# Kernel tuning notes

Hardware: AMD Instinct MI355X
Metric: run time of the kernel (lower is better)

The kernel has to match this reference:

```python
import jax, jax.numpy as jnp
import numpy as np

L, B, S, D = 8, 1, 4096, 2048
H, KVH, HD = 16, 2, 128
Q = 32
THETA = 1e6
MROPE = (16, 24, 24)  # mrope_section, sums to HD//2
EPS = 1e-6


def setup_inputs() -> dict:
    key = jax.random.key(0)
    ks = jax.random.split(key, 8)
    hidden_states = jax.random.normal(ks[0], (L, B, S, D), dtype=jnp.float32)
    ln_w = jax.random.uniform(ks[1], (L, D), dtype=jnp.float32, minval=0.5, maxval=1.5)
    q_w = jax.random.normal(ks[2], (L, D, H * HD), dtype=jnp.float32) * 0.02
    q_b = jax.random.normal(ks[3], (L, H * HD), dtype=jnp.float32) * 0.02
    k_w = jax.random.normal(ks[4], (L, D, KVH * HD), dtype=jnp.float32) * 0.02
    k_b = jax.random.normal(ks[5], (L, KVH * HD), dtype=jnp.float32) * 0.02
    position_ids = jax.random.randint(ks[6], (3, B, S), 0, S, dtype=jnp.int32)
    q_idx = jnp.sort(jax.random.randint(ks[7], (Q,), 0, S, dtype=jnp.int32))
    return {"hidden_states": hidden_states, "ln_w": ln_w, "q_w": q_w, "q_b": q_b,
            "k_w": k_w, "k_b": k_b, "position_ids": position_ids, "q_idx": q_idx}


def _rot_half(x):
    h = x.shape[-1] // 2
    return jnp.concatenate([-x[..., h:], x[..., :h]], axis=-1)


def _mrope_combine(t):
    # t: (3, B, S, HD). Split last dim per 2*mrope_section, chunk i taken from axis i%3.
    parts, off = [], 0
    for i, sec in enumerate(MROPE):
        w = 2 * sec
        parts.append(t[i % 3, :, :, off:off + w])
        off += w
    return jnp.concatenate(parts, axis=-1)[:, None, :, :]  # (B, 1, S, HD)


def reference(hidden_states, ln_w, q_w, q_b, k_w, k_b, position_ids, q_idx):
    # Rotary embeddings from 3D mRoPE position ids
    inv_freq = 1.0 / (THETA ** (jnp.arange(0, HD, 2, dtype=jnp.float32) / HD))  # (HD/2,)
    freqs = position_ids.astype(jnp.float32)[..., None] * inv_freq  # (3, B, S, HD/2)
    emb = jnp.concatenate([freqs, freqs], axis=-1)  # (3, B, S, HD)
    cos = _mrope_combine(jnp.cos(emb))  # (B, 1, S, HD)
    sin = _mrope_combine(jnp.sin(emb))
    cos_q = cos[:, :, q_idx, :]  # (B, 1, Q, HD)
    sin_q = sin[:, :, q_idx, :]
    # Eager causal mask sliced at query rows: (Q, S)
    mask_add = jnp.where(jnp.arange(S)[None, :] > q_idx[:, None], -1e9, 0.0).astype(jnp.float32)

    scale = 1.0 / np.sqrt(HD).astype(np.float32)

    def per_layer(hs, lw, qw, qb, kw, kb):
        # RMSNorm (input_layernorm)
        var = jnp.mean(jnp.square(hs), axis=-1, keepdims=True)
        x = hs * jax.lax.rsqrt(var + EPS) * lw  # (B, S, D)
        xq = x[:, q_idx, :]  # (B, Q, D)
        k = (jnp.einsum('bsd,de->bse', x, kw) + kb).reshape(B, S, KVH, HD).transpose(0, 2, 1, 3)
        q = (jnp.einsum('bqd,de->bqe', xq, qw) + qb).reshape(B, Q, H, HD).transpose(0, 2, 1, 3)
        k = jnp.repeat(k, H // KVH, axis=1)  # repeat_kv -> (B, H, S, HD)
        k = k * cos + _rot_half(k) * sin
        q = q * cos_q + _rot_half(q) * sin_q
        scores = jnp.einsum('bhqd,bhkd->bhqk', q, k) * scale  # (B, H, Q, S)
        scores = scores + mask_add[None, None]
        return jax.nn.softmax(scores.astype(jnp.float32), axis=-1)

    return jax.vmap(per_layer)(hidden_states, ln_w, q_w, q_b, k_w, k_b)  # (L, B, H, Q, S)
```

## Files before the change

### kernel.cpp

```cpp
#include <hip/hip_runtime.h>
#include <hip/hip_bf16.h>
#include <math.h>

#define LYR 8
#define SEQ 4096
#define DIM 2048
#define NH 16
#define HD 128
#define NQ 32
#define NKV 256
#define NQE 2048

typedef __attribute__((ext_vector_type(8))) short short8;
typedef __attribute__((ext_vector_type(4))) float f32x4;

#define WS_ABLOB 256
#define WS_COS   524544
#define WS_SIN   1048832
#define WS_PART  2097408
#define WS_W2    6291712
#define WS_KBLOB 10486016
#define WS_QROPE 18874624

__device__ __forceinline__ short f2bf(float x) {
  __hip_bfloat16 h = __float2bfloat16(x);
  return *(short*)&h;
}
__device__ __forceinline__ float bf2f(short s) {
  unsigned u = ((unsigned)(unsigned short)s) << 16;
  return __uint_as_float(u);
}

__device__ __forceinline__ void split1(float x, short& h, short& l) {
  unsigned b = __float_as_uint(x);
  h = (short)(b >> 16);
  float lo = x - __uint_as_float(b & 0xffff0000u);
  l = (short)((__float_as_uint(lo) + 0x8000u) >> 16);
}

#define GLOAD16(srcp, dstp) \
  __builtin_amdgcn_global_load_lds( \
      (const __attribute__((address_space(1))) unsigned int*)(srcp), \
      (__attribute__((address_space(3))) unsigned int*)(dstp), 16, 0, 0)

#define RBAR() asm volatile("s_waitcnt lgkmcnt(0)\n\ts_barrier" ::: "memory")

__global__ __launch_bounds__(256) void prep_kernel(
    const float* __restrict__ ln_w, const float* __restrict__ k_w,
    short* __restrict__ W2) {
  int kb = blockIdx.x, l = blockIdx.y, t = threadIdx.x;
  const float* kwl = k_w + (size_t)l * DIM * NKV;
  const float* lnl = ln_w + l * DIM;
  short* blob = W2 + (size_t)(l * 64 + kb) * 16384;
  #pragma unroll
  for (int i = 0; i < 4; ++i) {
    int p = t + i * 256;
    int fi = p >> 6, lane = p & 63;
    int n = fi * 16 + (lane & 15);
    int k0 = kb * 32 + (lane >> 4) * 8;
    short hi8[8], lo8[8];
    #pragma unroll
    for (int e = 0; e < 8; ++e) {
      float v = lnl[k0 + e] * kwl[(size_t)(k0 + e) * NKV + n];
      short h = f2bf(v);
      hi8[e] = h;
      lo8[e] = f2bf(v - bf2f(h));
    }
    *(short8*)(blob + p * 8) = *(short8*)hi8;
    *(short8*)(blob + 8192 + p * 8) = *(short8*)lo8;
  }
}

__global__ void cossin_kernel(const int* __restrict__ pos_ids,
                              float* __restrict__ cost, float* __restrict__ sint) {
  int idx = blockIdx.x * 256 + threadIdx.x;
  int s = idx >> 7, d = idx & 127;
  int t = (d < 32) ? 0 : (d < 80 ? 1 : 2);
  int j = d & 63;
  double invf = pow(1000000.0, -(double)j / 64.0);
  double ph = (double)pos_ids[t * SEQ + s] * invf;
  cost[idx] = (float)cos(ph);
  sint[idx] = (float)sin(ph);
}

__global__ __launch_bounds__(256) void xqt_kernel(
    const float* __restrict__ hs, const float* __restrict__ ln_w,
    const int* __restrict__ q_idx, short* __restrict__ Ablob) {
  __shared__ int qix[32];
  __shared__ float qir[32];
  int l = blockIdx.x, t = threadIdx.x;
  if (t < 32) qix[t] = q_idx[t];
  __syncthreads();
  {
    int row = t >> 3, seg = t & 7;
    const float* src = hs + ((size_t)l * SEQ + qix[row]) * DIM + seg * 256;
    float sq = 0.f;
    #pragma unroll
    for (int i = 0; i < 64; ++i) {
      float4 v = *(const float4*)(src + i * 4);
      sq = fmaf(v.x, v.x, fmaf(v.y, v.y, fmaf(v.z, v.z, fmaf(v.w, v.w, sq))));
    }
    sq += __shfl_xor(sq, 1);
    sq += __shfl_xor(sq, 2);
    sq += __shfl_xor(sq, 4);
    if (seg == 0) qir[row] = rsqrtf(sq / (float)DIM + 1e-6f);
  }
  __syncthreads();
  int lane = t & 63, g4 = t >> 6;
  short* base = Ablob + (size_t)l * 131072;
  int row = lane & 15, kgl = lane >> 4;
  for (int i = 0; i < 64; ++i) {
    int group = g4 * 64 + i;
    int kb = group >> 2, half = (group >> 1) & 1, mf = group & 1;
    int r = row + mf * 16;
    int k0 = kb * 32 + kgl * 8;
    const float* src = hs + ((size_t)l * SEQ + qix[r]) * DIM + k0;
    const float* lnp = ln_w + l * DIM + k0;
    float ir = qir[r];
    float4 v0 = *(const float4*)src;
    float4 v1 = *(const float4*)(src + 4);
    float4 w0 = *(const float4*)lnp;
    float4 w1 = *(const float4*)(lnp + 4);
    float av[8] = {v0.x*w0.x, v0.y*w0.y, v0.z*w0.z, v0.w*w0.w,
                   v1.x*w1.x, v1.y*w1.y, v1.z*w1.z, v1.w*w1.w};
    short o8[8];
    #pragma unroll
    for (int e = 0; e < 8; ++e) {
      float v = av[e] * ir;
      short hh, ll;
      split1(v, hh, ll);
      o8[e] = half ? ll : hh;
    }
    *(short8*)(base + group * 512 + lane * 8) = *(short8*)o8;
  }
}

__global__ __launch_bounds__(256) void kgemm_kernel(
    const float* __restrict__ hs, const short* __restrict__ W2,
    const float* __restrict__ k_b, const float* __restrict__ cost,
    const float* __restrict__ sint, short* __restrict__ Kblob) {
  __shared__ __align__(1024) char SM[65536];

  int t = threadIdx.x;
  int fid = blockIdx.x;
  int l = fid & 7, sb = fid >> 3;
  int s0 = sb * 64;
  int lane = t & 63, w = t >> 6;
  int fr = lane & 15, kg = lane >> 4;
  int arow = t >> 2, akg = t & 3;

  const float* hrow = hs + ((size_t)l * SEQ + s0 + arow) * DIM + akg * 8;
  const char* wbase = (const char*)(W2 + (size_t)l * 64 * 16384);
  const char* wfrag = wbase + w * 1024 + lane * 16;

  int awoff = (arow >> 4) * 1024 + (((akg * 16 + (arow & 15)) * 16) ^ (akg << 5));
  int aroff = (lane * 16) ^ ((lane >> 4) << 5);

  f32x4 acc[4][4];
  #pragma unroll
  for (int mf = 0; mf < 4; ++mf)
    #pragma unroll
    for (int nf = 0; nf < 4; ++nf) acc[mf][nf] = (f32x4){0.f, 0.f, 0.f, 0.f};
  float sq = 0.f;
  float4 rA0, rA1, rB0, rB1;
  short8 B0h[4], B0l[4], B1h[4], B1l[4];

  {
    #pragma unroll
    for (int nf = 0; nf < 4; ++nf) {
      B0h[nf] = *(const short8*)(wfrag + nf * 4096);
      B0l[nf] = *(const short8*)(wfrag + nf * 4096 + 16384);
    }
    float4 a0 = *(const float4*)(hrow);
    float4 a1 = *(const float4*)(hrow + 4);
    float av[8] = {a0.x, a0.y, a0.z, a0.w, a1.x, a1.y, a1.z, a1.w};
    short hi8[8], lo8[8];
    #pragma unroll
    for (int e = 0; e < 8; ++e) {
      sq = fmaf(av[e], av[e], sq);
      split1(av[e], hi8[e], lo8[e]);
    }
    *(short8*)(SM + awoff) = *(short8*)hi8;
    *(short8*)(SM + 4096 + awoff) = *(short8*)lo8;
    rA0 = *(const float4*)(hrow + 32);
    rA1 = *(const float4*)(hrow + 36);
  }
  RBAR();

#define KSTEP8(KB, CA0, CA1, NA0, NA1, UBH, UBL, PBH, PBL) do { \
    int buf_ = (KB) & 1; \
    const char* asb_ = SM + buf_ * 8192; \
    if ((KB) < 63) { \
      const char* bsrc_ = wfrag + (size_t)((KB) + 1) * 32768; \
      _Pragma("unroll") \
      for (int nf = 0; nf < 4; ++nf) { \
        PBH[nf] = *(const short8*)(bsrc_ + nf * 4096); \
        PBL[nf] = *(const short8*)(bsrc_ + nf * 4096 + 16384); \
      } \
    } \
    if ((KB) < 62) { \
      NA0 = *(const float4*)(hrow + ((KB) + 2) * 32); \
      NA1 = *(const float4*)(hrow + ((KB) + 2) * 32 + 4); \
    } \
    short8 ah_[4], al_[4]; \
    _Pragma("unroll") \
    for (int mf = 0; mf < 4; ++mf) { \
      ah_[mf] = *(const short8*)(asb_ + mf * 1024 + aroff); \
      al_[mf] = *(const short8*)(asb_ + 4096 + mf * 1024 + aroff); \
    } \
    __builtin_amdgcn_s_barrier(); \
    asm volatile("s_waitcnt lgkmcnt(0)" ::: "memory"); \
    __builtin_amdgcn_s_setprio(1); \
    _Pragma("unroll") \
    for (int nf = 0; nf < 2; ++nf) \
      _Pragma("unroll") \
      for (int mf = 0; mf < 4; ++mf) \
        acc[mf][nf] = __builtin_amdgcn_mfma_f32_16x16x32_bf16(ah_[mf], UBH[nf], acc[mf][nf], 0, 0, 0); \
    _Pragma("unroll") \
    for (int nf = 0; nf < 2; ++nf) \
      _Pragma("unroll") \
      for (int mf = 0; mf < 4; ++mf) \
        acc[mf][nf] = __builtin_amdgcn_mfma_f32_16x16x32_bf16(ah_[mf], UBL[nf], acc[mf][nf], 0, 0, 0); \
    _Pragma("unroll") \
    for (int nf = 0; nf < 2; ++nf) \
      _Pragma("unroll") \
      for (int mf = 0; mf < 4; ++mf) \
        acc[mf][nf] = __builtin_amdgcn_mfma_f32_16x16x32_bf16(al_[mf], UBH[nf], acc[mf][nf], 0, 0, 0); \
    __builtin_amdgcn_s_setprio(0); \
    __builtin_amdgcn_s_barrier(); \
    if ((KB) < 63) { \
      char* asn_ = SM + (buf_ ^ 1) * 8192; \
      float av_[8] = {CA0.x, CA0.y, CA0.z, CA0.w, CA1.x, CA1.y, CA1.z, CA1.w}; \
      short hi8_[8], lo8_[8]; \
      _Pragma("unroll") \
      for (int e = 0; e < 8; ++e) { \
        sq = fmaf(av_[e], av_[e], sq); \
        split1(av_[e], hi8_[e], lo8_[e]); \
      } \
      *(short8*)(asn_ + awoff) = *(short8*)hi8_; \
      *(short8*)(asn_ + 4096 + awoff) = *(short8*)lo8_; \
    } \
    __builtin_amdgcn_s_setprio(1); \
    _Pragma("unroll") \
    for (int nf = 2; nf < 4; ++nf) \
      _Pragma("unroll") \
      for (int mf = 0; mf < 4; ++mf) \
        acc[mf][nf] = __builtin_amdgcn_mfma_f32_16x16x32_bf16(ah_[mf], UBH[nf], acc[mf][nf], 0, 0, 0); \
    _Pragma("unroll") \
    for (int nf = 2; nf < 4; ++nf) \
      _Pragma("unroll") \
      for (int mf = 0; mf < 4; ++mf) \
        acc[mf][nf] = __builtin_amdgcn_mfma_f32_16x16x32_bf16(ah_[mf], UBL[nf], acc[mf][nf], 0, 0, 0); \
    _Pragma("unroll") \
    for (int nf = 2; nf < 4; ++nf) \
      _Pragma("unroll") \
      for (int mf = 0; mf < 4; ++mf) \
        acc[mf][nf] = __builtin_amdgcn_mfma_f32_16x16x32_bf16(al_[mf], UBH[nf], acc[mf][nf], 0, 0, 0); \
    __builtin_amdgcn_s_setprio(0); \
    asm volatile("s_waitcnt lgkmcnt(0)" ::: "memory"); \
    __builtin_amdgcn_s_barrier(); \
  } while (0)

  for (int kb2 = 0; kb2 < 32; ++kb2) {
    KSTEP8(2 * kb2,     rA0, rA1, rB0, rB1, B0h, B0l, B1h, B1l);
    KSTEP8(2 * kb2 + 1, rB0, rB1, rA0, rA1, B1h, B1l, B0h, B0l);
  }
#undef KSTEP8

  sq += __shfl_xor(sq, 1);
  sq += __shfl_xor(sq, 2);
  float* smf = (float*)SM;
  __syncthreads();
  if ((t & 3) == 0) smf[arow] = sq;
  __syncthreads();
  float irv[16];
  #pragma unroll
  for (int mf = 0; mf < 4; ++mf)
    #pragma unroll
    for (int r = 0; r < 4; ++r)
      irv[mf * 4 + r] = rsqrtf(smf[mf * 16 + kg * 4 + r] / (float)DIM + 1e-6f);
  __syncthreads();

  float* Kraw = smf;
  int j = w * 16 + fr;
  float bias0 = k_b[l * NKV + j];
  float bias1 = k_b[l * NKV + j + 64];
  float bias2 = k_b[l * NKV + j + 128];
  float bias3 = k_b[l * NKV + j + 192];
  #pragma unroll
  for (int mf = 0; mf < 4; ++mf) {
    #pragma unroll
    for (int r = 0; r < 4; ++r) {
      int row = mf * 16 + kg * 4 + r;
      int s = s0 + row;
      float ir = irv[mf * 4 + r];
      float v0 = acc[mf][0][r] * ir + bias0;
      float v1 = acc[mf][1][r] * ir + bias1;
      float v2 = acc[mf][2][r] * ir + bias2;
      float v3 = acc[mf][3][r] * ir + bias3;
      float cj = cost[s * HD + j], sj = sint[s * HD + j];
      float cj2 = cost[s * HD + j + 64], sj2 = sint[s * HD + j + 64];
      int sw = (row & 7) << 2;
      float* kr = Kraw + row * 256;
      kr[j ^ sw]           = v0 * cj - v1 * sj;
      kr[(j + 64) ^ sw]    = v1 * cj2 + v0 * sj2;
      kr[(j + 128) ^ sw]   = v2 * cj - v3 * sj;
      kr[(j + 192) ^ sw]   = v3 * cj2 + v2 * sj2;
    }
  }
  __syncthreads();

  int kc = sb >> 1, fb = (sb & 1) * 4;
  #pragma unroll
  for (int i = 0; i < 8; ++i) {
    int c = t + i * 256;
    int lc = c & 63, fl = (c >> 6) & 3, ts2 = (c >> 8) & 3, kv = c >> 10;
    int key = fl * 16 + (lc & 15);
    int d0 = kv * 128 + ts2 * 32 + (lc >> 4) * 8;
    int sw = (key & 7) << 2;
    float4 x0 = *(const float4*)(Kraw + key * 256 + (d0 ^ sw));
    float4 x1 = *(const float4*)(Kraw + key * 256 + ((d0 + 4) ^ sw));
    float av[8] = {x0.x, x0.y, x0.z, x0.w, x1.x, x1.y, x1.z, x1.w};
    short hi8[8], lo8[8];
    #pragma unroll
    for (int e = 0; e < 8; ++e) split1(av[e], hi8[e], lo8[e]);
    short* bb = Kblob + (size_t)((l * 2 + kv) * 32 + kc) * 32768
              + (size_t)((ts2 * 2 + 0) * 8 + fb + fl) * 512 + lc * 8;
    *(short8*)bb = *(short8*)hi8;
    *(short8*)(bb + 4096) = *(short8*)lo8;
  }
}

__global__ __launch_bounds__(256) void qgemm_kernel(
    const float* __restrict__ q_w, const short* __restrict__ Ablob,
    float* __restrict__ part) {
  __shared__ __align__(1024) char SM[65536];
  int t = threadIdx.x;
  int nc = blockIdx.x, ks = blockIdx.y, l = blockIdx.z;
  int lane = t & 63, w = t >> 6;
  int fr = lane & 15, kg = lane >> 4;
  const char* abase = (const char*)(Ablob + (size_t)l * 131072 + (size_t)ks * 16384);
  const float* qwl = q_w + (size_t)l * DIM * NQE;

  #pragma unroll
  for (int c = 0; c < 8; ++c) {
    int chunk = w * 8 + c;
    GLOAD16(abase + chunk * 1024 + lane * 16, SM + chunk * 1024);
  }
  #pragma unroll
  for (int c = 0; c < 4; ++c) {
    int r2 = (w * 4 + c) * 2;
    const char* src = (const char*)(qwl + (size_t)(ks * 256 + r2 + (lane >> 5)) * NQE + nc * 128) + (lane & 31) * 16;
    GLOAD16(src, SM + 32768 + (w * 4 + c) * 1024);
  }
  f32x4 acc[2][2];
  #pragma unroll
  for (int mf = 0; mf < 2; ++mf)
    #pragma unroll
    for (int nf = 0; nf < 2; ++nf) acc[mf][nf] = (f32x4){0.f, 0.f, 0.f, 0.f};
  __syncthreads();

  for (int ts = 0; ts < 8; ++ts) {
    int buf = ts & 1;
    if (ts < 7) {
      #pragma unroll
      for (int c = 0; c < 4; ++c) {
        int r2 = (w * 4 + c) * 2;
        const char* src = (const char*)(qwl + (size_t)(ks * 256 + (ts + 1) * 32 + r2 + (lane >> 5)) * NQE + nc * 128) + (lane & 31) * 16;
        GLOAD16(src, SM + 32768 + (buf ^ 1) * 16384 + (w * 4 + c) * 1024);
      }
    }
    short8 ah[2], al[2];
    #pragma unroll
    for (int mf = 0; mf < 2; ++mf) {
      ah[mf] = *(const short8*)(SM + ts * 4096 + mf * 1024 + lane * 16);
      al[mf] = *(const short8*)(SM + ts * 4096 + 2048 + mf * 1024 + lane * 16);
    }
    const float* bt = (const float*)(SM + 32768 + buf * 16384);
    short8 bh[2], bl[2];
    #pragma unroll
    for (int nf = 0; nf < 2; ++nf) {
      int c = w * 32 + nf * 16 + fr;
      short bh8[8], bl8[8];
      #pragma unroll
      for (int e = 0; e < 8; ++e) {
        float v = bt[(kg * 8 + e) * 128 + c];
        split1(v, bh8[e], bl8[e]);
      }
      bh[nf] = *(short8*)bh8;
      bl[nf] = *(short8*)bl8;
    }
    #pragma unroll
    for (int nf = 0; nf < 2; ++nf)
      #pragma unroll
      for (int mf = 0; mf < 2; ++mf)
        acc[mf][nf] = __builtin_amdgcn_mfma_f32_16x16x32_bf16(ah[mf], bh[nf], acc[mf][nf], 0, 0, 0);
    #pragma unroll
    for (int nf = 0; nf < 2; ++nf)
      #pragma unroll
      for (int mf = 0; mf < 2; ++mf)
        acc[mf][nf] = __builtin_amdgcn_mfma_f32_16x16x32_bf16(ah[mf], bl[nf], acc[mf][nf], 0, 0, 0);
    #pragma unroll
    for (int nf = 0; nf < 2; ++nf)
      #pragma unroll
      for (int mf = 0; mf < 2; ++mf)
        acc[mf][nf] = __builtin_amdgcn_mfma_f32_16x16x32_bf16(al[mf], bh[nf], acc[mf][nf], 0, 0, 0);
    __syncthreads();
  }

  #pragma unroll
  for (int mf = 0; mf < 2; ++mf) {
    #pragma unroll
    for (int r = 0; r < 4; ++r) {
      int row = mf * 16 + kg * 4 + r;
      float* prow = part + ((size_t)((ks * LYR + l) * NQ + row)) * NQE + nc * 128;
      #pragma unroll
      for (int nf = 0; nf < 2; ++nf) {
        int col = w * 32 + nf * 16 + fr;
        prow[col] = acc[mf][nf][r];
      }
    }
  }
}

__global__ __launch_bounds__(256) void qredrope_kernel(
    const float* __restrict__ part, const float* __restrict__ q_b,
    const float* __restrict__ cost, const float* __restrict__ sint,
    const int* __restrict__ q_idx, float* __restrict__ Qrope) {
  int p = blockIdx.x * 256 + threadIdx.x;
  int j = p & 63, q = (p >> 6) & 31, h = (p >> 11) & 15, l = p >> 15;
  int n1 = h * HD + j, n2 = n1 + 64;
  float v1 = q_b[l * NQE + n1];
  float v2 = q_b[l * NQE + n2];
  #pragma unroll
  for (int ks = 0; ks < 8; ++ks) {
    const float* pr = part + ((size_t)((ks * LYR + l) * NQ + q)) * NQE;
    v1 += pr[n1];
    v2 += pr[n2];
  }
  int s = q_idx[q];
  float c1 = cost[s * HD + j],      s1 = sint[s * HD + j];
  float c2 = cost[s * HD + j + 64], s2 = sint[s * HD + j + 64];
  const float SC = 0.088388347648318447f;
  float* orow = Qrope + ((size_t)(l * NH + h) * NQ + q) * HD;
  orow[j]      = (v1 * c1 - v2 * s1) * SC;
  orow[j + 64] = (v2 * c2 + v1 * s2) * SC;
}

__global__ __launch_bounds__(512) void attn_kernel(
    const float* __restrict__ Qrope, const short* __restrict__ Kblob,
    const int* __restrict__ q_idx, float* __restrict__ out) {
  __shared__ float smS[8 * 4104];
  __shared__ int qiv8[8];
  int t = threadIdx.x;
  int bid = blockIdx.x;
  int xcd = bid & 7, idx = bid >> 3;
  int pp = 2 * xcd + (idx >> 5);
  int l = pp >> 1, kv = pp & 1;
  int hh = (idx >> 2) & 7, qg = idx & 3;
  int h = kv * 8 + hh;
  int q0 = qg * 8;
  int lane = t & 63, w = t >> 6;
  int g = lane >> 4;

  if (t < 8) qiv8[t] = q_idx[q0 + t];

  short8 Ah[4], Al[4];
  {
    int arow = lane & 15, akg = lane >> 4;
    if (arow < 8) {
      const float* qr = Qrope + ((size_t)(l * NH + h) * NQ + q0 + arow) * HD + akg * 8;
      #pragma unroll
      for (int ts = 0; ts < 4; ++ts) {
        float4 a0 = *(const float4*)(qr + ts * 32);
        float4 a1 = *(const float4*)(qr + ts * 32 + 4);
        float av[8] = {a0.x, a0.y, a0.z, a0.w, a1.x, a1.y, a1.z, a1.w};
        short hi8[8], lo8[8];
        #pragma unroll
        for (int e = 0; e < 8; ++e) split1(av[e], hi8[e], lo8[e]);
        Ah[ts] = *(short8*)hi8;
        Al[ts] = *(short8*)lo8;
      }
    } else {
      short z8[8] = {0, 0, 0, 0, 0, 0, 0, 0};
      #pragma unroll
      for (int ts = 0; ts < 4; ++ts) { Ah[ts] = *(short8*)z8; Al[ts] = *(short8*)z8; }
    }
  }
  const short* kbase = Kblob + (size_t)((l * 2 + kv) * 32) * 32768 + w * 512 + lane * 8;
  short8 K0h[4], K0l[4], K1h[4], K1l[4];
  #pragma unroll
  for (int ts = 0; ts < 4; ++ts) {
    K0h[ts] = *(const short8*)(kbase + ts * 8192);
    K0l[ts] = *(const short8*)(kbase + ts * 8192 + 4096);
  }
  __syncthreads();

#define ACHUNK(KC, CH, CL, NH_, NL_) do { \
    if ((KC) < 31) { \
      const short* nb = kbase + (size_t)((KC) + 1) * 32768; \
      _Pragma("unroll") \
      for (int ts = 0; ts < 4; ++ts) { \
        NH_[ts] = *(const short8*)(nb + ts * 8192); \
        NL_[ts] = *(const short8*)(nb + ts * 8192 + 4096); \
      } \
    } \
    f32x4 acc = (f32x4){0.f, 0.f, 0.f, 0.f}; \
    _Pragma("unroll") \
    for (int ts = 0; ts < 4; ++ts) \
      acc = __builtin_amdgcn_mfma_f32_16x16x32_bf16(Ah[ts], CH[ts], acc, 0, 0, 0); \
    _Pragma("unroll") \
    for (int ts = 0; ts < 4; ++ts) \
      acc = __builtin_amdgcn_mfma_f32_16x16x32_bf16(Ah[ts], CL[ts], acc, 0, 0, 0); \
    _Pragma("unroll") \
    for (int ts = 0; ts < 4; ++ts) \
      acc = __builtin_amdgcn_mfma_f32_16x16x32_bf16(Al[ts], CH[ts], acc, 0, 0, 0); \
    if (g < 2) { \
      int key = (KC) * 128 + w * 16 + (lane & 15); \
      _Pragma("unroll") \
      for (int rr = 0; rr < 4; ++rr) { \
        int r8 = g * 4 + rr; \
        float v = (key > qiv8[r8]) ? -1e9f : acc[rr]; \
        smS[r8 * 4104 + key] = v; \
      } \
    } \
  } while (0)

  for (int kc2 = 0; kc2 < 16; ++kc2) {
    ACHUNK(2 * kc2,     K0h, K0l, K1h, K1l);
    ACHUNK(2 * kc2 + 1, K1h, K1l, K0h, K0l);
  }
#undef ACHUNK

  __syncthreads();
  int srow = w;
  float* S = smS + srow * 4104;
  float mx = -1e30f;
  #pragma unroll
  for (int c = 0; c < 16; ++c) {
    float4 x = *(const float4*)(S + c * 256 + lane * 4);
    mx = fmaxf(mx, fmaxf(fmaxf(x.x, x.y), fmaxf(x.z, x.w)));
  }
  #pragma unroll
  for (int off = 32; off >= 1; off >>= 1) mx = fmaxf(mx, __shfl_xor(mx, off));
  float sum = 0.f;
  #pragma unroll
  for (int c = 0; c < 16; ++c) {
    float4 x = *(const float4*)(S + c * 256 + lane * 4);
    x.x = __expf(x.x - mx); x.y = __expf(x.y - mx);
    x.z = __expf(x.z - mx); x.w = __expf(x.w - mx);
    sum += x.x + x.y + x.z + x.w;
    *(float4*)(S + c * 256 + lane * 4) = x;
  }
  #pragma unroll
  for (int off = 32; off >= 1; off >>= 1) sum += __shfl_xor(sum, off);
  float inv = 1.f / sum;
  float* orow = out + ((size_t)(l * NH + h) * NQ + q0 + srow) * SEQ;
  #pragma unroll
  for (int c = 0; c < 16; ++c) {
    float4 x = *(const float4*)(S + c * 256 + lane * 4);
    x.x *= inv; x.y *= inv; x.z *= inv; x.w *= inv;
    *(float4*)(orow + c * 256 + lane * 4) = x;
  }
}

extern "C" void kernel_launch(void* const* d_in, const int* in_sizes, int n_in,
                              void* d_out, int out_size, void* d_ws, size_t ws_size,
                              hipStream_t stream) {
  const float* hs   = (const float*)d_in[0];
  const float* ln_w = (const float*)d_in[1];
  const float* q_w  = (const float*)d_in[2];
  const float* q_b  = (const float*)d_in[3];
  const float* k_w  = (const float*)d_in[4];
  const float* k_b  = (const float*)d_in[5];
  const int* pos    = (const int*)d_in[6];
  const int* qidx   = (const int*)d_in[7];
  float* out = (float*)d_out;
  float* ws = (float*)d_ws;
  short* Ablob = (short*)(ws + WS_ABLOB);
  float* cost  = ws + WS_COS;
  float* sint  = ws + WS_SIN;
  float* part  = ws + WS_PART;
  short* W2    = (short*)(ws + WS_W2);
  short* Kblob = (short*)(ws + WS_KBLOB);
  float* Qrope = ws + WS_QROPE;

  prep_kernel<<<dim3(64, LYR), 256, 0, stream>>>(ln_w, k_w, W2);
  cossin_kernel<<<(SEQ * HD) / 256, 256, 0, stream>>>(pos, cost, sint);
  xqt_kernel<<<LYR, 256, 0, stream>>>(hs, ln_w, qidx, Ablob);
  kgemm_kernel<<<512, 256, 0, stream>>>(hs, W2, k_b, cost, sint, Kblob);
  qgemm_kernel<<<dim3(16, 8, LYR), 256, 0, stream>>>(q_w, Ablob, part);
  qredrope_kernel<<<1024, 256, 0, stream>>>(part, q_b, cost, sint, qidx, Qrope);
  attn_kernel<<<512, 512, 0, stream>>>(Qrope, Kblob, qidx, out);
}
```

Baseline: 260.7 us.

## Merge prep kernels into one launch and fuse Q reduction/RoPE into attention

Combines the weight-prep, cos/sin table and query-normalization kernels into a single launch that dispatches on block index. It also removes the separate Q split-K reduction and RoPE kernel by doing that work at the start of the attention kernel and staging the result in shared memory, so the Qrope buffer disappears. This cuts two launches and one global round trip. In exchange, each attention block recomputes its share of the Q reduction, which adds latency before the main loop.

```diff
diff --git a/kernel.cpp b/kernel.cpp
--- a/kernel.cpp
+++ b/kernel.cpp
@@ -20,7 +20,6 @@
 #define WS_PART  2097408
 #define WS_W2    6291712
 #define WS_KBLOB 10486016
-#define WS_QROPE 18874624
 
 __device__ __forceinline__ short f2bf(float x) {
   __hip_bfloat16 h = __float2bfloat16(x);
@@ -45,93 +44,90 @@
 
 #define RBAR() asm volatile("s_waitcnt lgkmcnt(0)\n\ts_barrier" ::: "memory")
 
-__global__ __launch_bounds__(256) void prep_kernel(
+__global__ __launch_bounds__(256) void pre_kernel(
     const float* __restrict__ ln_w, const float* __restrict__ k_w,
-    short* __restrict__ W2) {
-  int kb = blockIdx.x, l = blockIdx.y, t = threadIdx.x;
-  const float* kwl = k_w + (size_t)l * DIM * NKV;
-  const float* lnl = ln_w + l * DIM;
-  short* blob = W2 + (size_t)(l * 64 + kb) * 16384;
-  #pragma unroll
-  for (int i = 0; i < 4; ++i) {
-    int p = t + i * 256;
-    int fi = p >> 6, lane = p & 63;
-    int n = fi * 16 + (lane & 15);
-    int k0 = kb * 32 + (lane >> 4) * 8;
-    short hi8[8], lo8[8];
-    #pragma unroll
-    for (int e = 0; e < 8; ++e) {
-      float v = lnl[k0 + e] * kwl[(size_t)(k0 + e) * NKV + n];
-      short h = f2bf(v);
-      hi8[e] = h;
-      lo8[e] = f2bf(v - bf2f(h));
-    }
-    *(short8*)(blob + p * 8) = *(short8*)hi8;
-    *(short8*)(blob + 8192 + p * 8) = *(short8*)lo8;
-  }
-}
-
-__global__ void cossin_kernel(const int* __restrict__ pos_ids,
-                              float* __restrict__ cost, float* __restrict__ sint) {
-  int idx = blockIdx.x * 256 + threadIdx.x;
-  int s = idx >> 7, d = idx & 127;
-  int t = (d < 32) ? 0 : (d < 80 ? 1 : 2);
-  int j = d & 63;
-  double invf = pow(1000000.0, -(double)j / 64.0);
-  double ph = (double)pos_ids[t * SEQ + s] * invf;
-  cost[idx] = (float)cos(ph);
-  sint[idx] = (float)sin(ph);
-}
-
-__global__ __launch_bounds__(256) void xqt_kernel(
-    const float* __restrict__ hs, const float* __restrict__ ln_w,
-    const int* __restrict__ q_idx, short* __restrict__ Ablob) {
-  __shared__ int qix[32];
-  __shared__ float qir[32];
-  int l = blockIdx.x, t = threadIdx.x;
-  if (t < 32) qix[t] = q_idx[t];
-  __syncthreads();
-  {
-    int row = t >> 3, seg = t & 7;
-    const float* src = hs + ((size_t)l * SEQ + qix[row]) * DIM + seg * 256;
-    float sq = 0.f;
-    #pragma unroll
+    const float* __restrict__ hs, const int* __restrict__ pos_ids,
+    const int* __restrict__ q_idx, short* __restrict__ W2,
+    float* __restrict__ cost, float* __restrict__ sint,
+    short* __restrict__ Ablob) {
+  int bid = blockIdx.x, t = threadIdx.x;
+  if (bid < 512) {
+    int kb = bid & 63, l = bid >> 6;
+    const float* kwl = k_w + (size_t)l * DIM * NKV;
+    const float* lnl = ln_w + l * DIM;
+    short* blob = W2 + (size_t)(l * 64 + kb) * 16384;
+    #pragma unroll
+    for (int i = 0; i < 4; ++i) {
+      int p = t + i * 256;
+      int fi = p >> 6, lane = p & 63;
+      int n = fi * 16 + (lane & 15);
+      int k0 = kb * 32 + (lane >> 4) * 8;
+      short hi8[8], lo8[8];
+      #pragma unroll
+      for (int e = 0; e < 8; ++e) {
+        float v = lnl[k0 + e] * kwl[(size_t)(k0 + e) * NKV + n];
+        split1(v, hi8[e], lo8[e]);
+      }
+      *(short8*)(blob + p * 8) = *(short8*)hi8;
+      *(short8*)(blob + 8192 + p * 8) = *(short8*)lo8;
+    }
+  } else if (bid < 2560) {
+    int idx = (bid - 512) * 256 + t;
+    int s = idx >> 7, d = idx & 127;
+    int tc = (d < 32) ? 0 : (d < 80 ? 1 : 2);
+    int j = d & 63;
+    double invf = pow(1000000.0, -(double)j / 64.0);
+    double ph = (double)pos_ids[tc * SEQ + s] * invf;
+    cost[idx] = (float)cos(ph);
+    sint[idx] = (float)sin(ph);
+  } else {
+    __shared__ int qix[32];
+    __shared__ float qir[32];
+    int l = bid - 2560;
+    if (t < 32) qix[t] = q_idx[t];
+    __syncthreads();
+    {
+      int row = t >> 3, seg = t & 7;
+      const float* src = hs + ((size_t)l * SEQ + qix[row]) * DIM + seg * 256;
+      float sq = 0.f;
+      #pragma unroll
+      for (int i = 0; i < 64; ++i) {
+        float4 v = *(const float4*)(src + i * 4);
+        sq = fmaf(v.x, v.x, fmaf(v.y, v.y, fmaf(v.z, v.z, fmaf(v.w, v.w, sq))));
+      }
+      sq += __shfl_xor(sq, 1);
+      sq += __shfl_xor(sq, 2);
+      sq += __shfl_xor(sq, 4);
+      if (seg == 0) qir[row] = rsqrtf(sq / (float)DIM + 1e-6f);
+    }
+    __syncthreads();
+    int lane = t & 63, g4 = t >> 6;
+    short* base = Ablob + (size_t)l * 131072;
+    int row = lane & 15, kgl = lane >> 4;
     for (int i = 0; i < 64; ++i) {
-      float4 v = *(const float4*)(src + i * 4);
-      sq = fmaf(v.x, v.x, fmaf(v.y, v.y, fmaf(v.z, v.z, fmaf(v.w, v.w, sq))));
-    }
-    sq += __shfl_xor(sq, 1);
-    sq += __shfl_xor(sq, 2);
-    sq += __shfl_xor(sq, 4);
-    if (seg == 0) qir[row] = rsqrtf(sq / (float)DIM + 1e-6f);
-  }
-  __syncthreads();
-  int lane = t & 63, g4 = t >> 6;
-  short* base = Ablob + (size_t)l * 131072;
-  int row = lane & 15, kgl = lane >> 4;
-  for (int i = 0; i < 64; ++i) {
-    int group = g4 * 64 + i;
-    int kb = group >> 2, half = (group >> 1) & 1, mf = group & 1;
-    int r = row + mf * 16;
-    int k0 = kb * 32 + kgl * 8;
-    const float* src = hs + ((size_t)l * SEQ + qix[r]) * DIM + k0;
-    const float* lnp = ln_w + l * DIM + k0;
-    float ir = qir[r];
-    float4 v0 = *(const float4*)src;
-    float4 v1 = *(const float4*)(src + 4);
-    float4 w0 = *(const float4*)lnp;
-    float4 w1 = *(const float4*)(lnp + 4);
-    float av[8] = {v0.x*w0.x, v0.y*w0.y, v0.z*w0.z, v0.w*w0.w,
-                   v1.x*w1.x, v1.y*w1.y, v1.z*w1.z, v1.w*w1.w};
-    short o8[8];
-    #pragma unroll
-    for (int e = 0; e < 8; ++e) {
-      float v = av[e] * ir;
-      short hh, ll;
-      split1(v, hh, ll);
-      o8[e] = half ? ll : hh;
-    }
-    *(short8*)(base + group * 512 + lane * 8) = *(short8*)o8;
+      int group = g4 * 64 + i;
+      int kb = group >> 2, half = (group >> 1) & 1, mf = group & 1;
+      int r = row + mf * 16;
+      int k0 = kb * 32 + kgl * 8;
+      const float* src = hs + ((size_t)l * SEQ + qix[r]) * DIM + k0;
+      const float* lnp = ln_w + l * DIM + k0;
+      float ir = qir[r];
+      float4 v0 = *(const float4*)src;
+      float4 v1 = *(const float4*)(src + 4);
+      float4 w0 = *(const float4*)lnp;
+      float4 w1 = *(const float4*)(lnp + 4);
+      float av[8] = {v0.x*w0.x, v0.y*w0.y, v0.z*w0.z, v0.w*w0.w,
+                     v1.x*w1.x, v1.y*w1.y, v1.z*w1.z, v1.w*w1.w};
+      short o8[8];
+      #pragma unroll
+      for (int e = 0; e < 8; ++e) {
+        float v = av[e] * ir;
+        short hh, ll;
+        split1(v, hh, ll);
+        o8[e] = half ? ll : hh;
+      }
+      *(short8*)(base + group * 512 + lane * 8) = *(short8*)o8;
+    }
   }
 }
 
@@ -423,34 +419,13 @@
   }
 }
 
-__global__ __launch_bounds__(256) void qredrope_kernel(
+__global__ __launch_bounds__(512) void attn_kernel(
     const float* __restrict__ part, const float* __restrict__ q_b,
     const float* __restrict__ cost, const float* __restrict__ sint,
-    const int* __restrict__ q_idx, float* __restrict__ Qrope) {
-  int p = blockIdx.x * 256 + threadIdx.x;
-  int j = p & 63, q = (p >> 6) & 31, h = (p >> 11) & 15, l = p >> 15;
-  int n1 = h * HD + j, n2 = n1 + 64;
-  float v1 = q_b[l * NQE + n1];
-  float v2 = q_b[l * NQE + n2];
-  #pragma unroll
-  for (int ks = 0; ks < 8; ++ks) {
-    const float* pr = part + ((size_t)((ks * LYR + l) * NQ + q)) * NQE;
-    v1 += pr[n1];
-    v2 += pr[n2];
-  }
-  int s = q_idx[q];
-  float c1 = cost[s * HD + j],      s1 = sint[s * HD + j];
-  float c2 = cost[s * HD + j + 64], s2 = sint[s * HD + j + 64];
-  const float SC = 0.088388347648318447f;
-  float* orow = Qrope + ((size_t)(l * NH + h) * NQ + q) * HD;
-  orow[j]      = (v1 * c1 - v2 * s1) * SC;
-  orow[j + 64] = (v2 * c2 + v1 * s2) * SC;
-}
-
-__global__ __launch_bounds__(512) void attn_kernel(
-    const float* __restrict__ Qrope, const short* __restrict__ Kblob,
-    const int* __restrict__ q_idx, float* __restrict__ out) {
+    const short* __restrict__ Kblob, const int* __restrict__ q_idx,
+    float* __restrict__ out) {
   __shared__ float smS[8 * 4104];
+  __shared__ float smQ[8][128];
   __shared__ int qiv8[8];
   int t = threadIdx.x;
   int bid = blockIdx.x;
@@ -465,11 +440,32 @@
 
   if (t < 8) qiv8[t] = q_idx[q0 + t];
 
+  {
+    int row = t >> 6, j = t & 63;
+    int q = q0 + row;
+    int n1 = h * HD + j;
+    float v1 = q_b[l * NQE + n1];
+    float v2 = q_b[l * NQE + n1 + 64];
+    #pragma unroll
+    for (int ks = 0; ks < 8; ++ks) {
+      const float* pr = part + ((size_t)((ks * LYR + l) * NQ + q)) * NQE + n1;
+      v1 += pr[0];
+      v2 += pr[64];
+    }
+    int s = q_idx[q];
+    float c1 = cost[s * HD + j],      s1 = sint[s * HD + j];
+    float c2 = cost[s * HD + j + 64], s2 = sint[s * HD + j + 64];
+    const float SC = 0.088388347648318447f;
+    smQ[row][j]      = (v1 * c1 - v2 * s1) * SC;
+    smQ[row][j + 64] = (v2 * c2 + v1 * s2) * SC;
+  }
+  __syncthreads();
+
   short8 Ah[4], Al[4];
   {
     int arow = lane & 15, akg = lane >> 4;
     if (arow < 8) {
-      const float* qr = Qrope + ((size_t)(l * NH + h) * NQ + q0 + arow) * HD + akg * 8;
+      const float* qr = &smQ[arow][0] + akg * 8;
       #pragma unroll
       for (int ts = 0; ts < 4; ++ts) {
         float4 a0 = *(const float4*)(qr + ts * 32);
@@ -494,7 +490,6 @@
     K0h[ts] = *(const short8*)(kbase + ts * 8192);
     K0l[ts] = *(const short8*)(kbase + ts * 8192 + 4096);
   }
-  __syncthreads();
 
 #define ACHUNK(KC, CH, CL, NH_, NL_) do { \
     if ((KC) < 31) { \
@@ -583,13 +578,9 @@
   float* part  = ws + WS_PART;
   short* W2    = (short*)(ws + WS_W2);
   short* Kblob = (short*)(ws + WS_KBLOB);
-  float* Qrope = ws + WS_QROPE;
-
-  prep_kernel<<<dim3(64, LYR), 256, 0, stream>>>(ln_w, k_w, W2);
-  cossin_kernel<<<(SEQ * HD) / 256, 256, 0, stream>>>(pos, cost, sint);
-  xqt_kernel<<<LYR, 256, 0, stream>>>(hs, ln_w, qidx, Ablob);
+
+  pre_kernel<<<2568, 256, 0, stream>>>(ln_w, k_w, hs, pos, qidx, W2, cost, sint, Ablob);
   kgemm_kernel<<<512, 256, 0, stream>>>(hs, W2, k_b, cost, sint, Kblob);
   qgemm_kernel<<<dim3(16, 8, LYR), 256, 0, stream>>>(q_w, Ablob, part);
-  qredrope_kernel<<<1024, 256, 0, stream>>>(part, q_b, cost, sint, qidx, Qrope);
-  attn_kernel<<<512, 512, 0, stream>>>(Qrope, Kblob, qidx, out);
-}
+  attn_kernel<<<512, 512, 0, stream>>>(part, q_b, cost, sint, Kblob, qidx, out);
+}
```

New measurement: 258.2 us. No clear change (-1.0%).
